# Optimization experiments

Measured on AMD Instinct MI355X. Metric: run time of the kernel, lower is better.

## Reference

```python
import jax, jax.numpy as jnp
import numpy as np

B, N, HC, HH, K, D = 64, 300, 64, 64, 3, 10

def setup_inputs() -> dict:
    key = jax.random.key(0)
    ks = jax.random.split(key, 8)
    inp = {
        "z": jax.random.normal(ks[0], (B, N, HC), dtype=jnp.float32),
        "W_in": jax.random.normal(ks[1], (HH, HC), dtype=jnp.float32) / np.sqrt(HC),
        "b_in": jax.random.normal(ks[2], (HH,), dtype=jnp.float32) * 0.01,
        "W_out": jax.random.normal(ks[3], (HC * HC, HH), dtype=jnp.float32) / np.sqrt(HH),
        "b_out": jax.random.normal(ks[4], (HC * HC,), dtype=jnp.float32) * 0.01,
        "node_emb": jax.random.normal(ks[5], (N, D), dtype=jnp.float32),
        "weights_pool": jax.random.normal(ks[6], (D, K, HH, HH), dtype=jnp.float32) / np.sqrt(D * HH),
        "bias_pool": jax.random.normal(ks[7], (D, HH), dtype=jnp.float32) * 0.01,
    }
    return inp

def _agc(z, node_emb, weights_pool, bias_pool):
    n = node_emb.shape[0]
    # data-adaptive adjacency: softmax over rows of relu(E E^T)
    supports = jax.nn.softmax(jax.nn.relu(node_emb @ node_emb.T), axis=1)  # [N,N]
    support_set = [jnp.eye(n, dtype=z.dtype), supports]
    for _ in range(2, K):  # Chebyshev recursion T_k = 2A T_{k-1} - T_{k-2}
        support_set.append(2.0 * supports @ support_set[-1] - support_set[-2])
    S = jnp.stack(support_set, axis=0)  # [K,N,N]
    weights = jnp.einsum('nd,dkio->nkio', node_emb, weights_pool)  # [N,K,HH,HH]
    bias = node_emb @ bias_pool  # [N,HH]
    x_g = jnp.einsum('knm,bmc->bnkc', S, z)  # [B,N,K,HH]
    return jnp.einsum('bnki,nkio->bno', x_g, weights) + bias

def reference(z, W_in, b_in, W_out, b_out, node_emb, weights_pool, bias_pool):
    h = jax.nn.relu(z @ W_in.T + b_in)                  # [B,N,HH]
    h = _agc(h, node_emb, weights_pool, bias_pool)      # [B,N,HH]
    out = (h @ W_out.T + b_out).reshape(B, N, HC, HC)   # [B,N,HC,HC]
    return jnp.tanh(out)
```

## Files before the change

kernel.cpp:

```cpp
#include <hip/hip_runtime.h>
#include <hip/hip_bf16.h>

#define BB 64
#define NN 300
#define HH 64
#define RTOT (BB*NN)
#define KIO  (3*HH*HH)
#define JOUT (HH*HH)

typedef __attribute__((ext_vector_type(8))) _Float16 f16x8;
typedef __attribute__((ext_vector_type(4))) float floatx4;

__device__ inline float tanh_fast(float x) {
    float e = __expf(2.f * x);
    return 1.f - 2.f * __builtin_amdgcn_rcpf(e + 1.f);
}

__global__ __launch_bounds__(256) void k_adjacency(const float* __restrict__ E,
                                                   float* __restrict__ A) {
    __shared__ float sE[16];
    __shared__ float row[NN];
    __shared__ float red[256];
    int n = blockIdx.x, tid = threadIdx.x;
    if (tid < 10) sE[tid] = E[n*10 + tid];
    __syncthreads();
    float lmax = -1e30f;
    for (int m = tid; m < NN; m += 256) {
        float s = 0.f;
        #pragma unroll
        for (int d = 0; d < 10; ++d) s += sE[d] * E[m*10 + d];
        s = fmaxf(s, 0.f);
        row[m] = s;
        lmax = fmaxf(lmax, s);
    }
    red[tid] = lmax; __syncthreads();
    for (int off = 128; off > 0; off >>= 1) {
        if (tid < off) red[tid] = fmaxf(red[tid], red[tid+off]);
        __syncthreads();
    }
    float mx = red[0]; __syncthreads();
    float lsum = 0.f;
    for (int m = tid; m < NN; m += 256) {
        float e = __expf(row[m] - mx);
        row[m] = e;
        lsum += e;
    }
    red[tid] = lsum; __syncthreads();
    for (int off = 128; off > 0; off >>= 1) {
        if (tid < off) red[tid] += red[tid+off];
        __syncthreads();
    }
    float inv = 1.f / red[0];
    for (int m = tid; m < NN; m += 256) A[n*NN + m] = row[m] * inv;
}

__global__ __launch_bounds__(256) void k_cheb(const float* __restrict__ A,
                                              float* __restrict__ T2) {
    int idx = blockIdx.x*256 + threadIdx.x;
    if (idx >= NN*NN) return;
    int n = idx / NN, m = idx % NN;
    float s = 0.f;
    for (int l = 0; l < NN; ++l) s += A[n*NN + l] * A[l*NN + m];
    T2[idx] = 2.f*s - (n == m ? 1.f : 0.f);
}

__global__ __launch_bounds__(256) void k_node_weights(const float* __restrict__ E,
                                                      const float* __restrict__ pool,
                                                      float* __restrict__ Wn) {
    int idx = blockIdx.x*256 + threadIdx.x;
    int n = idx / KIO, kio = idx % KIO;
    float s = 0.f;
    #pragma unroll
    for (int d = 0; d < 10; ++d) s += E[n*10 + d] * pool[d*KIO + kio];
    Wn[idx] = s;
}

__global__ __launch_bounds__(256) void k_node_bias(const float* __restrict__ E,
                                                   const float* __restrict__ bpool,
                                                   float* __restrict__ bN) {
    int idx = blockIdx.x*256 + threadIdx.x;
    int n = idx >> 6, o = idx & 63;
    float s = 0.f;
    #pragma unroll
    for (int d = 0; d < 10; ++d) s += E[n*10 + d] * bpool[d*64 + o];
    bN[idx] = s;
}

__global__ __launch_bounds__(256) void k_cvt_wout(const float* __restrict__ W,
                                                  _Float16* __restrict__ Wh) {
    int idx = blockIdx.x*256 + threadIdx.x;
    Wh[idx] = (_Float16)W[idx];
}

__global__ __launch_bounds__(256) void k_in_proj(const float* __restrict__ z,
                                                 const float* __restrict__ Win,
                                                 const float* __restrict__ bin,
                                                 float* __restrict__ h) {
    __shared__ float Wt[64*68];
    __shared__ float zl[64*66];
    int tx = threadIdx.x, ty = threadIdx.y;
    int tid = ty*16 + tx;
    int r0 = blockIdx.y * 64;
    for (int e = tid; e < 4096; e += 256) {
        int o = e >> 6, c = e & 63;
        Wt[c*68 + o] = Win[e];
        zl[o*66 + c] = z[(r0 + o)*64 + c];
    }
    __syncthreads();
    float4 bo = *(const float4*)&bin[tx*4];
    float acc[4][4];
    #pragma unroll
    for (int s = 0; s < 4; ++s) { acc[s][0]=bo.x; acc[s][1]=bo.y; acc[s][2]=bo.z; acc[s][3]=bo.w; }
    const float* zr = &zl[(ty*4)*66];
    for (int c = 0; c < 64; ++c) {
        float4 w = *(const float4*)&Wt[c*68 + tx*4];
        float z0 = zr[c], z1 = zr[66+c], z2 = zr[132+c], z3 = zr[198+c];
        acc[0][0] += z0*w.x; acc[0][1] += z0*w.y; acc[0][2] += z0*w.z; acc[0][3] += z0*w.w;
        acc[1][0] += z1*w.x; acc[1][1] += z1*w.y; acc[1][2] += z1*w.z; acc[1][3] += z1*w.w;
        acc[2][0] += z2*w.x; acc[2][1] += z2*w.y; acc[2][2] += z2*w.z; acc[2][3] += z2*w.w;
        acc[3][0] += z3*w.x; acc[3][1] += z3*w.y; acc[3][2] += z3*w.z; acc[3][3] += z3*w.w;
    }
    #pragma unroll
    for (int s = 0; s < 4; ++s) {
        float4 v = make_float4(fmaxf(acc[s][0],0.f), fmaxf(acc[s][1],0.f),
                               fmaxf(acc[s][2],0.f), fmaxf(acc[s][3],0.f));
        *(float4*)&h[(r0 + ty*4 + s)*64 + tx*4] = v;
    }
}

__global__ __launch_bounds__(256) void k_spatial2(const float* __restrict__ A,
                                                  const float* __restrict__ T2,
                                                  const float* __restrict__ h,
                                                  float* __restrict__ xg1,
                                                  float* __restrict__ xg2) {
    int tid = threadIdx.x;
    int c = tid & 63;
    int w = __builtin_amdgcn_readfirstlane(tid >> 6);
    int b = blockIdx.y;
    int r0 = blockIdx.x * 20 + w * 5;
    const float* S;
    float* dst;
    if (r0 < NN) {
        S   = A   + (size_t)r0 * NN;
        dst = xg1 + ((size_t)b * NN + r0) * 64 + c;
    } else {
        S   = T2  + (size_t)(r0 - NN) * NN;
        dst = xg2 + ((size_t)b * NN + (r0 - NN)) * 64 + c;
    }
    const float* hb = h + (size_t)b * NN * 64 + c;
    float a0 = 0.f, a1 = 0.f, a2 = 0.f, a3 = 0.f, a4 = 0.f;
    for (int m = 0; m < NN; m += 4) {
        float4 s0 = *(const float4*)(S + 0*NN + m);
        float4 s1 = *(const float4*)(S + 1*NN + m);
        float4 s2 = *(const float4*)(S + 2*NN + m);
        float4 s3 = *(const float4*)(S + 3*NN + m);
        float4 s4 = *(const float4*)(S + 4*NN + m);
        float h0 = hb[(m+0)*64];
        float h1 = hb[(m+1)*64];
        float h2 = hb[(m+2)*64];
        float h3 = hb[(m+3)*64];
        a0 = fmaf(s0.x,h0,a0); a0 = fmaf(s0.y,h1,a0); a0 = fmaf(s0.z,h2,a0); a0 = fmaf(s0.w,h3,a0);
        a1 = fmaf(s1.x,h0,a1); a1 = fmaf(s1.y,h1,a1); a1 = fmaf(s1.z,h2,a1); a1 = fmaf(s1.w,h3,a1);
        a2 = fmaf(s2.x,h0,a2); a2 = fmaf(s2.y,h1,a2); a2 = fmaf(s2.z,h2,a2); a2 = fmaf(s2.w,h3,a2);
        a3 = fmaf(s3.x,h0,a3); a3 = fmaf(s3.y,h1,a3); a3 = fmaf(s3.z,h2,a3); a3 = fmaf(s3.w,h3,a3);
        a4 = fmaf(s4.x,h0,a4); a4 = fmaf(s4.y,h1,a4); a4 = fmaf(s4.z,h2,a4); a4 = fmaf(s4.w,h3,a4);
    }
    dst[0*64] = a0;
    dst[1*64] = a1;
    dst[2*64] = a2;
    dst[3*64] = a3;
    dst[4*64] = a4;
}

__global__ __launch_bounds__(256) void k_node_mm(const float* __restrict__ h,
                                                 const float* __restrict__ xg1,
                                                 const float* __restrict__ xg2,
                                                 const float* __restrict__ Wn,
                                                 const float* __restrict__ bN,
                                                 _Float16* __restrict__ h2h) {
    __shared__ float Wnl[192*64];
    __shared__ float xgl[8][192];
    int tid = threadIdx.x;
    int o = tid & 63, ty = tid >> 6;
    int n = blockIdx.x, b0 = blockIdx.y*8;
    for (int e = tid; e < 12288; e += 256) Wnl[e] = Wn[(size_t)n*KIO + e];
    for (int e = tid; e < 8*192; e += 256) {
        int bb = e / 192, ki = e % 192;
        int k = ki >> 6, i = ki & 63;
        const float* src = (k == 0) ? h : ((k == 1) ? xg1 : xg2);
        xgl[bb][ki] = src[((b0+bb)*NN + n)*64 + i];
    }
    __syncthreads();
    float bias = bN[n*64 + o];
    for (int bb = ty; bb < 8; bb += 4) {
        float acc = bias;
        for (int ki = 0; ki < 192; ++ki) acc += xgl[bb][ki] * Wnl[ki*64 + o];
        h2h[((b0+bb)*NN + n)*64 + o] = (_Float16)acc;
    }
}

__global__ __launch_bounds__(256) void k_out_proj_mfma(const _Float16* __restrict__ h2h,
                                                       const _Float16* __restrict__ Wh,
                                                       const float* __restrict__ bout,
                                                       float* __restrict__ out) {
    int tid  = threadIdx.x;
    int wave = tid >> 6, lane = tid & 63;
    int quad = lane >> 4, lr = lane & 15;
    int m0 = blockIdx.y*128 + (wave >> 1)*64;
    int n0 = blockIdx.x*128 + (wave & 1)*64;
    floatx4 acc[4][4] = {};
    const _Float16* Aptr = h2h + (size_t)(m0 + lr)*64 + quad*8;
    const _Float16* Bptr = Wh  + (size_t)(n0 + lr)*64 + quad*8;
    #pragma unroll
    for (int ks = 0; ks < 2; ++ks) {
        f16x8 a[4], b[4];
        #pragma unroll
        for (int f = 0; f < 4; ++f) {
            a[f] = *(const f16x8*)(Aptr + (size_t)f*16*64 + ks*32);
            b[f] = *(const f16x8*)(Bptr + (size_t)f*16*64 + ks*32);
        }
        #pragma unroll
        for (int mf = 0; mf < 4; ++mf)
            #pragma unroll
            for (int nf = 0; nf < 4; ++nf)
                acc[mf][nf] = __builtin_amdgcn_mfma_f32_16x16x32_f16(a[mf], b[nf], acc[mf][nf], 0, 0, 0);
    }
    #pragma unroll
    for (int nf = 0; nf < 4; ++nf) {
        int col = n0 + nf*16 + lr;
        float bj = bout[col];
        #pragma unroll
        for (int mf = 0; mf < 4; ++mf) {
            int row = m0 + mf*16 + quad*4;
            #pragma unroll
            for (int r = 0; r < 4; ++r) {
                float v = tanh_fast(acc[mf][nf][r] + bj);
                __builtin_nontemporal_store(v, &out[(size_t)(row + r)*JOUT + col]);
            }
        }
    }
}

extern "C" void kernel_launch(void* const* d_in, const int* in_sizes, int n_in,
                              void* d_out, int out_size, void* d_ws, size_t ws_size,
                              hipStream_t stream) {
    const float* z     = (const float*)d_in[0];
    const float* Win   = (const float*)d_in[1];
    const float* bin   = (const float*)d_in[2];
    const float* Wout  = (const float*)d_in[3];
    const float* bout  = (const float*)d_in[4];
    const float* E     = (const float*)d_in[5];
    const float* pool  = (const float*)d_in[6];
    const float* bpool = (const float*)d_in[7];
    float* out = (float*)d_out;

    float* ws  = (float*)d_ws;
    float* A   = ws;
    float* T2  = A   + 90000;
    float* Wn  = T2  + 90000;
    float* bN  = Wn  + 3686400;
    float* h   = bN  + 19200;
    float* xg1 = h   + 1228800;
    float* xg2 = xg1 + 1228800;
    _Float16* h2h  = (_Float16*)(xg2 + 1228800);
    _Float16* Wouth = h2h + 1228800;

    k_adjacency   <<<NN, 256, 0, stream>>>(E, A);
    k_cheb        <<<(NN*NN + 255)/256, 256, 0, stream>>>(A, T2);
    k_node_weights<<<14400, 256, 0, stream>>>(E, pool, Wn);
    k_node_bias   <<<75, 256, 0, stream>>>(E, bpool, bN);
    k_cvt_wout    <<<1024, 256, 0, stream>>>(Wout, Wouth);
    k_in_proj     <<<dim3(1, RTOT/64), dim3(16,16), 0, stream>>>(z, Win, bin, h);
    k_spatial2    <<<dim3(30, BB), 256, 0, stream>>>(A, T2, h, xg1, xg2);
    k_node_mm     <<<dim3(NN, 8), 256, 0, stream>>>(h, xg1, xg2, Wn, bN, h2h);
    k_out_proj_mfma<<<dim3(JOUT/128, RTOT/128), 256, 0, stream>>>(h2h, Wouth, bout, out);
}
```

Measured before the change: 469.6 us.

## Replace dense Chebyshev T2 matrix with recursive A·(A·h) and merge prep kernels

Drops the naive O(N^3) A·A kernel that built T2. The second support term is now computed as 2·A·(A·h) − h through two sequential spatial passes. The adjacency, input projection, node bias, W_out fp16 conversion and node-weight kernels are merged into one launch that branches on block index, which cuts launch overhead and lets the independent work overlap. The trade-off is that the spatial stage becomes two dependent launches and the merged kernel's shared-memory footprint applies to every block.

```diff
diff --git a/kernel.cpp b/kernel.cpp
--- a/kernel.cpp
+++ b/kernel.cpp
@@ -16,137 +16,115 @@
     return 1.f - 2.f * __builtin_amdgcn_rcpf(e + 1.f);
 }
 
-__global__ __launch_bounds__(256) void k_adjacency(const float* __restrict__ E,
-                                                   float* __restrict__ A) {
-    __shared__ float sE[16];
-    __shared__ float row[NN];
-    __shared__ float red[256];
-    int n = blockIdx.x, tid = threadIdx.x;
-    if (tid < 10) sE[tid] = E[n*10 + tid];
-    __syncthreads();
-    float lmax = -1e30f;
-    for (int m = tid; m < NN; m += 256) {
+__global__ __launch_bounds__(256) void k_pre(const float* __restrict__ E,
+                                             const float* __restrict__ z,
+                                             const float* __restrict__ Win,
+                                             const float* __restrict__ bin,
+                                             const float* __restrict__ Wout,
+                                             const float* __restrict__ pool,
+                                             const float* __restrict__ bpool,
+                                             float* __restrict__ A,
+                                             float* __restrict__ h,
+                                             float* __restrict__ Wn,
+                                             float* __restrict__ bN,
+                                             _Float16* __restrict__ Wh) {
+    __shared__ float smem[8576];
+    int bid = blockIdx.x, tid = threadIdx.x;
+
+    if (bid < 300) {
+        float* sE  = smem;
+        float* row = smem + 16;
+        float* red = smem + 320;
+        int n = bid;
+        if (tid < 10) sE[tid] = E[n*10 + tid];
+        __syncthreads();
+        float lmax = -1e30f;
+        for (int m = tid; m < NN; m += 256) {
+            float s = 0.f;
+            #pragma unroll
+            for (int d = 0; d < 10; ++d) s += sE[d] * E[m*10 + d];
+            s = fmaxf(s, 0.f);
+            row[m] = s;
+            lmax = fmaxf(lmax, s);
+        }
+        red[tid] = lmax; __syncthreads();
+        for (int off = 128; off > 0; off >>= 1) {
+            if (tid < off) red[tid] = fmaxf(red[tid], red[tid+off]);
+            __syncthreads();
+        }
+        float mx = red[0]; __syncthreads();
+        float lsum = 0.f;
+        for (int m = tid; m < NN; m += 256) {
+            float e = __expf(row[m] - mx);
+            row[m] = e;
+            lsum += e;
+        }
+        red[tid] = lsum; __syncthreads();
+        for (int off = 128; off > 0; off >>= 1) {
+            if (tid < off) red[tid] += red[tid+off];
+            __syncthreads();
+        }
+        float inv = 1.f / red[0];
+        for (int m = tid; m < NN; m += 256) A[n*NN + m] = row[m] * inv;
+    } else if (bid < 600) {
+        float* Wt = smem;
+        float* zl = smem + 4352;
+        int tx = tid & 15, ty = tid >> 4;
+        int r0 = (bid - 300) * 64;
+        for (int e = tid; e < 4096; e += 256) {
+            int o = e >> 6, c = e & 63;
+            Wt[c*68 + o] = Win[e];
+            zl[o*66 + c] = z[(size_t)(r0 + o)*64 + c];
+        }
+        __syncthreads();
+        float4 bo = *(const float4*)&bin[tx*4];
+        float acc[4][4];
+        #pragma unroll
+        for (int s = 0; s < 4; ++s) { acc[s][0]=bo.x; acc[s][1]=bo.y; acc[s][2]=bo.z; acc[s][3]=bo.w; }
+        const float* zr = &zl[(ty*4)*66];
+        for (int c = 0; c < 64; ++c) {
+            float4 w = *(const float4*)&Wt[c*68 + tx*4];
+            float z0 = zr[c], z1 = zr[66+c], z2 = zr[132+c], z3 = zr[198+c];
+            acc[0][0] += z0*w.x; acc[0][1] += z0*w.y; acc[0][2] += z0*w.z; acc[0][3] += z0*w.w;
+            acc[1][0] += z1*w.x; acc[1][1] += z1*w.y; acc[1][2] += z1*w.z; acc[1][3] += z1*w.w;
+            acc[2][0] += z2*w.x; acc[2][1] += z2*w.y; acc[2][2] += z2*w.z; acc[2][3] += z2*w.w;
+            acc[3][0] += z3*w.x; acc[3][1] += z3*w.y; acc[3][2] += z3*w.z; acc[3][3] += z3*w.w;
+        }
+        #pragma unroll
+        for (int s = 0; s < 4; ++s) {
+            float4 v = make_float4(fmaxf(acc[s][0],0.f), fmaxf(acc[s][1],0.f),
+                                   fmaxf(acc[s][2],0.f), fmaxf(acc[s][3],0.f));
+            *(float4*)&h[(size_t)(r0 + ty*4 + s)*64 + tx*4] = v;
+        }
+    } else if (bid < 675) {
+        int idx = (bid - 600)*256 + tid;
+        int n = idx >> 6, o = idx & 63;
         float s = 0.f;
         #pragma unroll
-        for (int d = 0; d < 10; ++d) s += sE[d] * E[m*10 + d];
-        s = fmaxf(s, 0.f);
-        row[m] = s;
-        lmax = fmaxf(lmax, s);
-    }
-    red[tid] = lmax; __syncthreads();
-    for (int off = 128; off > 0; off >>= 1) {
-        if (tid < off) red[tid] = fmaxf(red[tid], red[tid+off]);
-        __syncthreads();
-    }
-    float mx = red[0]; __syncthreads();
-    float lsum = 0.f;
-    for (int m = tid; m < NN; m += 256) {
-        float e = __expf(row[m] - mx);
-        row[m] = e;
-        lsum += e;
-    }
-    red[tid] = lsum; __syncthreads();
-    for (int off = 128; off > 0; off >>= 1) {
-        if (tid < off) red[tid] += red[tid+off];
-        __syncthreads();
-    }
-    float inv = 1.f / red[0];
-    for (int m = tid; m < NN; m += 256) A[n*NN + m] = row[m] * inv;
-}
-
-__global__ __launch_bounds__(256) void k_cheb(const float* __restrict__ A,
-                                              float* __restrict__ T2) {
-    int idx = blockIdx.x*256 + threadIdx.x;
-    if (idx >= NN*NN) return;
-    int n = idx / NN, m = idx % NN;
-    float s = 0.f;
-    for (int l = 0; l < NN; ++l) s += A[n*NN + l] * A[l*NN + m];
-    T2[idx] = 2.f*s - (n == m ? 1.f : 0.f);
-}
-
-__global__ __launch_bounds__(256) void k_node_weights(const float* __restrict__ E,
-                                                      const float* __restrict__ pool,
-                                                      float* __restrict__ Wn) {
-    int idx = blockIdx.x*256 + threadIdx.x;
-    int n = idx / KIO, kio = idx % KIO;
-    float s = 0.f;
-    #pragma unroll
-    for (int d = 0; d < 10; ++d) s += E[n*10 + d] * pool[d*KIO + kio];
-    Wn[idx] = s;
-}
-
-__global__ __launch_bounds__(256) void k_node_bias(const float* __restrict__ E,
-                                                   const float* __restrict__ bpool,
-                                                   float* __restrict__ bN) {
-    int idx = blockIdx.x*256 + threadIdx.x;
-    int n = idx >> 6, o = idx & 63;
-    float s = 0.f;
-    #pragma unroll
-    for (int d = 0; d < 10; ++d) s += E[n*10 + d] * bpool[d*64 + o];
-    bN[idx] = s;
-}
-
-__global__ __launch_bounds__(256) void k_cvt_wout(const float* __restrict__ W,
-                                                  _Float16* __restrict__ Wh) {
-    int idx = blockIdx.x*256 + threadIdx.x;
-    Wh[idx] = (_Float16)W[idx];
-}
-
-__global__ __launch_bounds__(256) void k_in_proj(const float* __restrict__ z,
-                                                 const float* __restrict__ Win,
-                                                 const float* __restrict__ bin,
-                                                 float* __restrict__ h) {
-    __shared__ float Wt[64*68];
-    __shared__ float zl[64*66];
-    int tx = threadIdx.x, ty = threadIdx.y;
-    int tid = ty*16 + tx;
-    int r0 = blockIdx.y * 64;
-    for (int e = tid; e < 4096; e += 256) {
-        int o = e >> 6, c = e & 63;
-        Wt[c*68 + o] = Win[e];
-        zl[o*66 + c] = z[(r0 + o)*64 + c];
-    }
-    __syncthreads();
-    float4 bo = *(const float4*)&bin[tx*4];
-    float acc[4][4];
-    #pragma unroll
-    for (int s = 0; s < 4; ++s) { acc[s][0]=bo.x; acc[s][1]=bo.y; acc[s][2]=bo.z; acc[s][3]=bo.w; }
-    const float* zr = &zl[(ty*4)*66];
-    for (int c = 0; c < 64; ++c) {
-        float4 w = *(const float4*)&Wt[c*68 + tx*4];
-        float z0 = zr[c], z1 = zr[66+c], z2 = zr[132+c], z3 = zr[198+c];
-        acc[0][0] += z0*w.x; acc[0][1] += z0*w.y; acc[0][2] += z0*w.z; acc[0][3] += z0*w.w;
-        acc[1][0] += z1*w.x; acc[1][1] += z1*w.y; acc[1][2] += z1*w.z; acc[1][3] += z1*w.w;
-        acc[2][0] += z2*w.x; acc[2][1] += z2*w.y; acc[2][2] += z2*w.z; acc[2][3] += z2*w.w;
-        acc[3][0] += z3*w.x; acc[3][1] += z3*w.y; acc[3][2] += z3*w.z; acc[3][3] += z3*w.w;
-    }
-    #pragma unroll
-    for (int s = 0; s < 4; ++s) {
-        float4 v = make_float4(fmaxf(acc[s][0],0.f), fmaxf(acc[s][1],0.f),
-                               fmaxf(acc[s][2],0.f), fmaxf(acc[s][3],0.f));
-        *(float4*)&h[(r0 + ty*4 + s)*64 + tx*4] = v;
-    }
-}
-
-__global__ __launch_bounds__(256) void k_spatial2(const float* __restrict__ A,
-                                                  const float* __restrict__ T2,
+        for (int d = 0; d < 10; ++d) s += E[n*10 + d] * bpool[d*64 + o];
+        bN[idx] = s;
+    } else if (bid < 1699) {
+        int idx = (bid - 675)*256 + tid;
+        Wh[idx] = (_Float16)Wout[idx];
+    } else {
+        int idx = (bid - 1699)*256 + tid;
+        int n = idx / KIO, kio = idx % KIO;
+        float s = 0.f;
+        #pragma unroll
+        for (int d = 0; d < 10; ++d) s += E[n*10 + d] * pool[d*KIO + kio];
+        Wn[idx] = s;
+    }
+}
+
+__global__ __launch_bounds__(256) void k_spatialA(const float* __restrict__ A,
                                                   const float* __restrict__ h,
-                                                  float* __restrict__ xg1,
-                                                  float* __restrict__ xg2) {
+                                                  float* __restrict__ xg1) {
     int tid = threadIdx.x;
     int c = tid & 63;
     int w = __builtin_amdgcn_readfirstlane(tid >> 6);
     int b = blockIdx.y;
     int r0 = blockIdx.x * 20 + w * 5;
-    const float* S;
-    float* dst;
-    if (r0 < NN) {
-        S   = A   + (size_t)r0 * NN;
-        dst = xg1 + ((size_t)b * NN + r0) * 64 + c;
-    } else {
-        S   = T2  + (size_t)(r0 - NN) * NN;
-        dst = xg2 + ((size_t)b * NN + (r0 - NN)) * 64 + c;
-    }
+    const float* S = A + (size_t)r0 * NN;
     const float* hb = h + (size_t)b * NN * 64 + c;
     float a0 = 0.f, a1 = 0.f, a2 = 0.f, a3 = 0.f, a4 = 0.f;
     for (int m = 0; m < NN; m += 4) {
@@ -165,11 +143,45 @@
         a3 = fmaf(s3.x,h0,a3); a3 = fmaf(s3.y,h1,a3); a3 = fmaf(s3.z,h2,a3); a3 = fmaf(s3.w,h3,a3);
         a4 = fmaf(s4.x,h0,a4); a4 = fmaf(s4.y,h1,a4); a4 = fmaf(s4.z,h2,a4); a4 = fmaf(s4.w,h3,a4);
     }
-    dst[0*64] = a0;
-    dst[1*64] = a1;
-    dst[2*64] = a2;
-    dst[3*64] = a3;
-    dst[4*64] = a4;
+    float* dst = xg1 + ((size_t)b * NN + r0) * 64 + c;
+    dst[0*64] = a0; dst[1*64] = a1; dst[2*64] = a2; dst[3*64] = a3; dst[4*64] = a4;
+}
+
+__global__ __launch_bounds__(256) void k_spatialB(const float* __restrict__ A,
+                                                  const float* __restrict__ xg1,
+                                                  const float* __restrict__ h,
+                                                  float* __restrict__ xg2) {
+    int tid = threadIdx.x;
+    int c = tid & 63;
+    int w = __builtin_amdgcn_readfirstlane(tid >> 6);
+    int b = blockIdx.y;
+    int r0 = blockIdx.x * 20 + w * 5;
+    const float* S = A + (size_t)r0 * NN;
+    const float* xb = xg1 + (size_t)b * NN * 64 + c;
+    float a0 = 0.f, a1 = 0.f, a2 = 0.f, a3 = 0.f, a4 = 0.f;
+    for (int m = 0; m < NN; m += 4) {
+        float4 s0 = *(const float4*)(S + 0*NN + m);
+        float4 s1 = *(const float4*)(S + 1*NN + m);
+        float4 s2 = *(const float4*)(S + 2*NN + m);
+        float4 s3 = *(const float4*)(S + 3*NN + m);
+        float4 s4 = *(const float4*)(S + 4*NN + m);
+        float x0 = xb[(m+0)*64];
+        float x1 = xb[(m+1)*64];
+        float x2 = xb[(m+2)*64];
+        float x3 = xb[(m+3)*64];
+        a0 = fmaf(s0.x,x0,a0); a0 = fmaf(s0.y,x1,a0); a0 = fmaf(s0.z,x2,a0); a0 = fmaf(s0.w,x3,a0);
+        a1 = fmaf(s1.x,x0,a1); a1 = fmaf(s1.y,x1,a1); a1 = fmaf(s1.z,x2,a1); a1 = fmaf(s1.w,x3,a1);
+        a2 = fmaf(s2.x,x0,a2); a2 = fmaf(s2.y,x1,a2); a2 = fmaf(s2.z,x2,a2); a2 = fmaf(s2.w,x3,a2);
+        a3 = fmaf(s3.x,x0,a3); a3 = fmaf(s3.y,x1,a3); a3 = fmaf(s3.z,x2,a3); a3 = fmaf(s3.w,x3,a3);
+        a4 = fmaf(s4.x,x0,a4); a4 = fmaf(s4.y,x1,a4); a4 = fmaf(s4.z,x2,a4); a4 = fmaf(s4.w,x3,a4);
+    }
+    const float* hb = h   + ((size_t)b * NN + r0) * 64 + c;
+    float*       dst = xg2 + ((size_t)b * NN + r0) * 64 + c;
+    dst[0*64] = 2.f*a0 - hb[0*64];
+    dst[1*64] = 2.f*a1 - hb[1*64];
+    dst[2*64] = 2.f*a2 - hb[2*64];
+    dst[3*64] = 2.f*a3 - hb[3*64];
+    dst[4*64] = 2.f*a4 - hb[4*64];
 }
 
 __global__ __launch_bounds__(256) void k_node_mm(const float* __restrict__ h,
@@ -256,22 +268,18 @@
 
     float* ws  = (float*)d_ws;
     float* A   = ws;
-    float* T2  = A   + 90000;
-    float* Wn  = T2  + 90000;
+    float* Wn  = A   + 90000;
     float* bN  = Wn  + 3686400;
     float* h   = bN  + 19200;
     float* xg1 = h   + 1228800;
     float* xg2 = xg1 + 1228800;
-    _Float16* h2h  = (_Float16*)(xg2 + 1228800);
+    _Float16* h2h   = (_Float16*)(xg2 + 1228800);
     _Float16* Wouth = h2h + 1228800;
 
-    k_adjacency   <<<NN, 256, 0, stream>>>(E, A);
-    k_cheb        <<<(NN*NN + 255)/256, 256, 0, stream>>>(A, T2);
-    k_node_weights<<<14400, 256, 0, stream>>>(E, pool, Wn);
-    k_node_bias   <<<75, 256, 0, stream>>>(E, bpool, bN);
-    k_cvt_wout    <<<1024, 256, 0, stream>>>(Wout, Wouth);
-    k_in_proj     <<<dim3(1, RTOT/64), dim3(16,16), 0, stream>>>(z, Win, bin, h);
-    k_spatial2    <<<dim3(30, BB), 256, 0, stream>>>(A, T2, h, xg1, xg2);
-    k_node_mm     <<<dim3(NN, 8), 256, 0, stream>>>(h, xg1, xg2, Wn, bN, h2h);
+    k_pre      <<<16099, 256, 0, stream>>>(E, z, Win, bin, Wout, pool, bpool,
+                                           A, h, Wn, bN, Wouth);
+    k_spatialA <<<dim3(15, BB), 256, 0, stream>>>(A, h, xg1);
+    k_spatialB <<<dim3(15, BB), 256, 0, stream>>>(A, xg1, h, xg2);
+    k_node_mm  <<<dim3(NN, 8), 256, 0, stream>>>(h, xg1, xg2, Wn, bN, h2h);
     k_out_proj_mfma<<<dim3(JOUT/128, RTOT/128), 256, 0, stream>>>(h2h, Wouth, bout, out);
 }
```

After: 454.6 us. 1.03x faster.
